# Kernel tuning notes

Measured on AMD Instinct MI355X. Metric: run time of the kernel, lower is better.

The kernel has to match this reference:

```python
import jax, jax.numpy as jnp
from jax import lax
import numpy as np

CHUNK = 1024  # query-chunk size; per-chunk intermediate is [B, CHUNK, M]


def _nn_min_sqdist(x, y):
    """For each point in x [B,N,D], squared distance to nearest point in y [B,M,D] -> [B,N].
    Computed in chunks over N so the full [B,N,M] matrix is never materialized."""
    B, N, D = x.shape
    y2 = jnp.sum(y * y, axis=-1)  # [B,M]
    n_chunks = N // CHUNK
    xs = x.reshape(B, n_chunks, CHUNK, D).transpose(1, 0, 2, 3)  # [n_chunks,B,CHUNK,D]

    def body(carry, xc):
        x2 = jnp.sum(xc * xc, axis=-1)  # [B,CHUNK]
        xy = jnp.einsum('bcd,bmd->bcm', xc, y)  # [B,CHUNK,M]
        d = x2[..., None] + y2[:, None, :] - 2.0 * xy
        return carry, jnp.min(d, axis=-1)  # [B,CHUNK]

    _, mins = lax.scan(body, None, xs)  # [n_chunks,B,CHUNK]
    return mins.transpose(1, 0, 2).reshape(B, N)


def setup_inputs() -> dict:
    key = jax.random.key(0)
    k1, k2 = jax.random.split(key)
    input1 = jax.random.normal(k1, (8, 16384, 3), dtype=jnp.float32)
    input2 = jax.random.normal(k2, (8, 16384, 3), dtype=jnp.float32)
    return {"input1": input1, "input2": input2}


def reference(input1, input2):
    # Chamfer nearest-neighbor squared distances, both directions.
    dist1 = _nn_min_sqdist(input1, input2)  # [B,N1]
    dist2 = _nn_min_sqdist(input2, input1)  # [B,N2]
    return (dist1, dist2)
```

## Files before the change

kernel.cpp:

```cpp
#include <hip/hip_runtime.h>


#define NB        8
#define NPTS      16384
#define TILE      2048
#define THREADS   256
#define PPT       2
#define PTS_PER_BLOCK (THREADS * PPT)

__global__ __launch_bounds__(THREADS, 2)
void nnd_kernel(const float* __restrict__ x1,
                const float* __restrict__ x2,
                float* __restrict__ out)
{
    constexpr int blocks_per_dir = (NB * NPTS) / PTS_PER_BLOCK;
    constexpr int chunks_per_batch = NPTS / PTS_PER_BLOCK;

    const int bid   = blockIdx.x;
    const int dir   = bid / blocks_per_dir;
    const int rem   = bid % blocks_per_dir;
    const int batch = rem / chunks_per_batch;
    const int chunk = rem % chunks_per_batch;

    const float* __restrict__ xq = (dir == 0) ? x1 : x2;
    const float* __restrict__ yr = (dir == 0) ? x2 : x1;
    const float* __restrict__ xb = xq + (size_t)batch * NPTS * 3;
    const float* __restrict__ yb = yr + (size_t)batch * NPTS * 3;
    float* __restrict__ ob = out + (size_t)dir * NB * NPTS
                                 + (size_t)batch * NPTS
                                 + (size_t)chunk * PTS_PER_BLOCK;

    __shared__ float4 ytile[TILE];

    const int t  = threadIdx.x;
    const int i0 = chunk * PTS_PER_BLOCK + t;
    const int i1 = i0 + THREADS;

    const float ax = xb[3 * i0 + 0], ay = xb[3 * i0 + 1], az = xb[3 * i0 + 2];
    const float bx = xb[3 * i1 + 0], by = xb[3 * i1 + 1], bz = xb[3 * i1 + 2];
    const float sa = ax * ax + ay * ay + az * az;
    const float sb = bx * bx + by * by + bz * bz;
    const float nax = -2.0f * ax, nay = -2.0f * ay, naz = -2.0f * az;
    const float nbx = -2.0f * bx, nby = -2.0f * by, nbz = -2.0f * bz;

    float mA0 = INFINITY, mA1 = INFINITY;
    float mB0 = INFINITY, mB1 = INFINITY;

    for (int tile0 = 0; tile0 < NPTS; tile0 += TILE) {
        for (int k = t; k < TILE; k += THREADS) {
            const float* yp = yb + 3 * (size_t)(tile0 + k);
            const float a = yp[0], b = yp[1], c = yp[2];
            ytile[k] = make_float4(a, b, c, a * a + b * b + c * c);
        }
        __syncthreads();

#pragma unroll 2
        for (int j = 0; j < TILE; j += 4) {
            const float4 p0 = ytile[j + 0];
            const float4 p1 = ytile[j + 1];
            const float4 p2 = ytile[j + 2];
            const float4 p3 = ytile[j + 3];

            const float dA0 = fmaf(nax, p0.x, fmaf(nay, p0.y, fmaf(naz, p0.z, p0.w)));
            const float dA1 = fmaf(nax, p1.x, fmaf(nay, p1.y, fmaf(naz, p1.z, p1.w)));
            const float dA2 = fmaf(nax, p2.x, fmaf(nay, p2.y, fmaf(naz, p2.z, p2.w)));
            const float dA3 = fmaf(nax, p3.x, fmaf(nay, p3.y, fmaf(naz, p3.z, p3.w)));

            const float dB0 = fmaf(nbx, p0.x, fmaf(nby, p0.y, fmaf(nbz, p0.z, p0.w)));
            const float dB1 = fmaf(nbx, p1.x, fmaf(nby, p1.y, fmaf(nbz, p1.z, p1.w)));
            const float dB2 = fmaf(nbx, p2.x, fmaf(nby, p2.y, fmaf(nbz, p2.z, p2.w)));
            const float dB3 = fmaf(nbx, p3.x, fmaf(nby, p3.y, fmaf(nbz, p3.z, p3.w)));

            mA0 = fminf(fminf(dA0, dA1), mA0);
            mA1 = fminf(fminf(dA2, dA3), mA1);
            mB0 = fminf(fminf(dB0, dB1), mB0);
            mB1 = fminf(fminf(dB2, dB3), mB1);
        }
        __syncthreads();
    }

    ob[t]           = sa + fminf(mA0, mA1);
    ob[t + THREADS] = sb + fminf(mB0, mB1);
}

extern "C" void kernel_launch(void* const* d_in, const int* in_sizes, int n_in,
                              void* d_out, int out_size, void* d_ws, size_t ws_size,
                              hipStream_t stream) {
    const float* x1 = (const float*)d_in[0];
    const float* x2 = (const float*)d_in[1];
    float* out = (float*)d_out;

    const int total_blocks = 2 * (NB * NPTS) / PTS_PER_BLOCK;
    nnd_kernel<<<dim3(total_blocks), dim3(THREADS), 0, stream>>>(x1, x2, out);
}
```

Measured before the change: 405.9 us.

## Split reference set across blocks, use packed FMA and min3, merge via atomicMin

The reference point set is split into four segments handled by separate blocks, and partial minima are merged with an unsigned-int atomicMin on distances clamped to be non-negative, after a memset of the output to 0xFF. Each thread now handles four query points. The shared-memory tile moves to a structure-of-arrays layout so v_pk_fma_f32 can evaluate two reference points per instruction, and v_min3_f32 folds the reduction. This raises ALU throughput per instruction and keeps the block count up despite the larger per-thread work, at the cost of an extra memset launch, atomic traffic, and clamping slightly negative distances to zero, which differs from the reference.

```diff
diff --git a/kernel.cpp b/kernel.cpp
--- a/kernel.cpp
+++ b/kernel.cpp
@@ -1,26 +1,42 @@
 #include <hip/hip_runtime.h>
 
 
-#define NB        8
-#define NPTS      16384
-#define TILE      2048
-#define THREADS   256
-#define PPT       2
-#define PTS_PER_BLOCK (THREADS * PPT)
+#define NB      8
+#define NPTS    16384
+#define THREADS 256
+#define PPT     4
+#define QPB     (THREADS * PPT)
+#define TILE    2048
+#define NSEG    4
+#define YSEG    (NPTS / NSEG)
 
-__global__ __launch_bounds__(THREADS, 2)
+typedef float v2f __attribute__((ext_vector_type(2)));
+
+__device__ __forceinline__ v2f pk_fma(v2f a, v2f b, v2f c) {
+    v2f d;
+    asm("v_pk_fma_f32 %0, %1, %2, %3" : "=v"(d) : "v"(a), "v"(b), "v"(c));
+    return d;
+}
+
+__device__ __forceinline__ float min3f(float a, float b, float c) {
+    float d;
+    asm("v_min3_f32 %0, %1, %2, %3" : "=v"(d) : "v"(a), "v"(b), "v"(c));
+    return d;
+}
+
+__global__ __launch_bounds__(THREADS, 4)
 void nnd_kernel(const float* __restrict__ x1,
                 const float* __restrict__ x2,
                 float* __restrict__ out)
 {
-    constexpr int blocks_per_dir = (NB * NPTS) / PTS_PER_BLOCK;
-    constexpr int chunks_per_batch = NPTS / PTS_PER_BLOCK;
-
+    constexpr int chunks = NPTS / QPB;
     const int bid   = blockIdx.x;
-    const int dir   = bid / blocks_per_dir;
-    const int rem   = bid % blocks_per_dir;
-    const int batch = rem / chunks_per_batch;
-    const int chunk = rem % chunks_per_batch;
+    const int yseg  = bid % NSEG;
+    const int rem1  = bid / NSEG;
+    const int chunk = rem1 % chunks;
+    const int rem2  = rem1 / chunks;
+    const int batch = rem2 % NB;
+    const int dir   = rem2 / NB;
 
     const float* __restrict__ xq = (dir == 0) ? x1 : x2;
     const float* __restrict__ yr = (dir == 0) ? x2 : x1;
@@ -28,59 +44,74 @@
     const float* __restrict__ yb = yr + (size_t)batch * NPTS * 3;
     float* __restrict__ ob = out + (size_t)dir * NB * NPTS
                                  + (size_t)batch * NPTS
-                                 + (size_t)chunk * PTS_PER_BLOCK;
+                                 + (size_t)chunk * QPB;
 
-    __shared__ float4 ytile[TILE];
+    __shared__ __align__(16) float ysx[TILE];
+    __shared__ __align__(16) float ysy[TILE];
+    __shared__ __align__(16) float ysz[TILE];
+    __shared__ __align__(16) float ysw[TILE];
 
-    const int t  = threadIdx.x;
-    const int i0 = chunk * PTS_PER_BLOCK + t;
-    const int i1 = i0 + THREADS;
+    const int t = threadIdx.x;
 
-    const float ax = xb[3 * i0 + 0], ay = xb[3 * i0 + 1], az = xb[3 * i0 + 2];
-    const float bx = xb[3 * i1 + 0], by = xb[3 * i1 + 1], bz = xb[3 * i1 + 2];
-    const float sa = ax * ax + ay * ay + az * az;
-    const float sb = bx * bx + by * by + bz * bz;
-    const float nax = -2.0f * ax, nay = -2.0f * ay, naz = -2.0f * az;
-    const float nbx = -2.0f * bx, nby = -2.0f * by, nbz = -2.0f * bz;
+    v2f nx[PPT], ny[PPT], nz[PPT];
+    float sx[PPT];
+    float a0[PPT], a1[PPT];
+#pragma unroll
+    for (int p = 0; p < PPT; ++p) {
+        const int q = chunk * QPB + t + p * THREADS;
+        const float qx = xb[3 * q + 0], qy = xb[3 * q + 1], qz = xb[3 * q + 2];
+        sx[p] = qx * qx + qy * qy + qz * qz;
+        const float mx = -2.0f * qx, my = -2.0f * qy, mz = -2.0f * qz;
+        nx[p] = (v2f){mx, mx};
+        ny[p] = (v2f){my, my};
+        nz[p] = (v2f){mz, mz};
+        a0[p] = INFINITY;
+        a1[p] = INFINITY;
+    }
 
-    float mA0 = INFINITY, mA1 = INFINITY;
-    float mB0 = INFINITY, mB1 = INFINITY;
+    const int segbase = yseg * YSEG;
 
-    for (int tile0 = 0; tile0 < NPTS; tile0 += TILE) {
+    for (int tile0 = 0; tile0 < YSEG; tile0 += TILE) {
         for (int k = t; k < TILE; k += THREADS) {
-            const float* yp = yb + 3 * (size_t)(tile0 + k);
+            const float* yp = yb + 3 * (size_t)(segbase + tile0 + k);
             const float a = yp[0], b = yp[1], c = yp[2];
-            ytile[k] = make_float4(a, b, c, a * a + b * b + c * c);
+            ysx[k] = a; ysy[k] = b; ysz[k] = c;
+            ysw[k] = a * a + b * b + c * c;
         }
         __syncthreads();
 
 #pragma unroll 2
         for (int j = 0; j < TILE; j += 4) {
-            const float4 p0 = ytile[j + 0];
-            const float4 p1 = ytile[j + 1];
-            const float4 p2 = ytile[j + 2];
-            const float4 p3 = ytile[j + 3];
+            const v2f x01 = *(const v2f*)&ysx[j];
+            const v2f x23 = *(const v2f*)&ysx[j + 2];
+            const v2f y01 = *(const v2f*)&ysy[j];
+            const v2f y23 = *(const v2f*)&ysy[j + 2];
+            const v2f z01 = *(const v2f*)&ysz[j];
+            const v2f z23 = *(const v2f*)&ysz[j + 2];
+            const v2f w01 = *(const v2f*)&ysw[j];
+            const v2f w23 = *(const v2f*)&ysw[j + 2];
 
-            const float dA0 = fmaf(nax, p0.x, fmaf(nay, p0.y, fmaf(naz, p0.z, p0.w)));
-            const float dA1 = fmaf(nax, p1.x, fmaf(nay, p1.y, fmaf(naz, p1.z, p1.w)));
-            const float dA2 = fmaf(nax, p2.x, fmaf(nay, p2.y, fmaf(naz, p2.z, p2.w)));
-            const float dA3 = fmaf(nax, p3.x, fmaf(nay, p3.y, fmaf(naz, p3.z, p3.w)));
-
-            const float dB0 = fmaf(nbx, p0.x, fmaf(nby, p0.y, fmaf(nbz, p0.z, p0.w)));
-            const float dB1 = fmaf(nbx, p1.x, fmaf(nby, p1.y, fmaf(nbz, p1.z, p1.w)));
-            const float dB2 = fmaf(nbx, p2.x, fmaf(nby, p2.y, fmaf(nbz, p2.z, p2.w)));
-            const float dB3 = fmaf(nbx, p3.x, fmaf(nby, p3.y, fmaf(nbz, p3.z, p3.w)));
-
-            mA0 = fminf(fminf(dA0, dA1), mA0);
-            mA1 = fminf(fminf(dA2, dA3), mA1);
-            mB0 = fminf(fminf(dB0, dB1), mB0);
-            mB1 = fminf(fminf(dB2, dB3), mB1);
+#pragma unroll
+            for (int p = 0; p < PPT; ++p) {
+                v2f t01 = pk_fma(nz[p], z01, w01);
+                t01 = pk_fma(ny[p], y01, t01);
+                t01 = pk_fma(nx[p], x01, t01);
+                v2f t23 = pk_fma(nz[p], z23, w23);
+                t23 = pk_fma(ny[p], y23, t23);
+                t23 = pk_fma(nx[p], x23, t23);
+                a0[p] = min3f(t01.x, t01.y, a0[p]);
+                a1[p] = min3f(t23.x, t23.y, a1[p]);
+            }
         }
         __syncthreads();
     }
 
-    ob[t]           = sa + fminf(mA0, mA1);
-    ob[t + THREADS] = sb + fminf(mB0, mB1);
+#pragma unroll
+    for (int p = 0; p < PPT; ++p) {
+        float d = sx[p] + fminf(a0[p], a1[p]);
+        d = fmaxf(d, 0.0f);
+        atomicMin((unsigned int*)&ob[t + p * THREADS], __float_as_uint(d));
+    }
 }
 
 extern "C" void kernel_launch(void* const* d_in, const int* in_sizes, int n_in,
@@ -90,6 +121,8 @@
     const float* x2 = (const float*)d_in[1];
     float* out = (float*)d_out;
 
-    const int total_blocks = 2 * (NB * NPTS) / PTS_PER_BLOCK;
+    hipMemsetAsync(out, 0xFF, (size_t)out_size * sizeof(float), stream);
+
+    constexpr int total_blocks = 2 * NB * (NPTS / QPB) * NSEG;
     nnd_kernel<<<dim3(total_blocks), dim3(THREADS), 0, stream>>>(x1, x2, out);
 }
```

After: 359.9 us. 1.13x faster.
